# Kernel optimization log

Hardware: AMD Instinct MI355X
Metric: run time of the kernel (lower is better)

Reference implementation:

```python
import jax, jax.numpy as jnp
import numpy as np

# Fixed supermask = [3, 4, 16, 28, 0, 0, 0, 3]:
#   preproc: relu(Linear x3); l1 = GCN(x); l2 = GCN(l1); l3 = GCN(l2);
#   out = relu(Linear z3((l1+l2+l3)/3))
HIDDEN = 64


def gcn_conv(h, W, b, src, dst, norm, n_nodes):
    # PyG GCNConv: h' = scatter_add(norm * (hW)[src] -> dst) + b
    hw = h @ W                                  # [N, F]
    msg = hw[src] * norm[:, None]               # gather + scale  [E+N, F]
    agg = jax.ops.segment_sum(msg, dst, num_segments=n_nodes)
    return agg + b


def setup_inputs() -> dict:
    key = jax.random.key(0)
    ks = jax.random.split(key, 12)
    N, E, NFEAT, NCLASS = 100000, 1000000, 256, 40
    x = jax.random.normal(ks[0], (N, NFEAT), dtype=jnp.float32)
    edge_index = jax.random.randint(ks[1], (2, E), 0, N, dtype=jnp.int64)
    s = 1.0 / np.sqrt(NFEAT)
    h = 1.0 / np.sqrt(HIDDEN)
    return {
        "x": x,
        "edge_index": edge_index,
        "Wx": jax.random.uniform(ks[2], (NFEAT, HIDDEN), jnp.float32, -s, s),
        "bx": jnp.zeros((HIDDEN,), jnp.float32),
        "W1": jax.random.uniform(ks[3], (HIDDEN, HIDDEN), jnp.float32, -h, h),
        "b1": jnp.zeros((HIDDEN,), jnp.float32),
        "W2": jax.random.uniform(ks[4], (HIDDEN, HIDDEN), jnp.float32, -h, h),
        "b2": jnp.zeros((HIDDEN,), jnp.float32),
        "W3": jax.random.uniform(ks[5], (HIDDEN, HIDDEN), jnp.float32, -h, h),
        "b3": jnp.zeros((HIDDEN,), jnp.float32),
        "Wz": jax.random.uniform(ks[6], (HIDDEN, NCLASS), jnp.float32, -h, h),
        "bz": jnp.zeros((NCLASS,), jnp.float32),
    }


def reference(x, edge_index, Wx, bx, W1, b1, W2, b2, W3, b3, Wz, bz):
    n = x.shape[0]
    # add self-loops (PyG GCNConv default)
    loop = jnp.arange(n, dtype=edge_index.dtype)
    src = jnp.concatenate([edge_index[0], loop])
    dst = jnp.concatenate([edge_index[1], loop])
    deg = jax.ops.segment_sum(jnp.ones_like(dst, dtype=x.dtype), dst, num_segments=n)
    dinv = jnp.where(deg > 0, jax.lax.rsqrt(deg), 0.0)
    norm = dinv[src] * dinv[dst]                 # [E+N]

    h0 = jax.nn.relu(x @ Wx + bx)                # x_3(relu) o x3(Linear)
    l1 = gcn_conv(h0, W1, b1, src, dst, norm, n)
    l2 = gcn_conv(l1, W2, b2, src, dst, norm, n)
    l3 = gcn_conv(l2, W3, b3, src, dst, norm, n)
    z = (l1 + l2 + l3) / 3.0
    return jax.nn.relu(z @ Wz + bz)
```

## Files before the change

### kernel.cpp

```cpp
#include <hip/hip_runtime.h>

#define NFEAT 256
#define HID 64
#define NCLASS 40
#define EPB 4096
#define BCAP 8192

typedef _Float16 half8 __attribute__((ext_vector_type(8)));
typedef float floatx4 __attribute__((ext_vector_type(4)));

__device__ __forceinline__ void gld_lds16(const _Float16* g, _Float16* l) {
    __builtin_amdgcn_global_load_lds(
        (const __attribute__((address_space(1))) void*)g,
        (__attribute__((address_space(3))) void*)l, 16, 0, 0);
}

__global__ __launch_bounds__(256) void k_bin(const int* __restrict__ src, const int* __restrict__ dst,
                                             int* __restrict__ bcur, int* __restrict__ bwords,
                                             int nbuckets, int E, int nbin,
                                             const float* __restrict__ W1, const float* __restrict__ W2,
                                             const float* __restrict__ W3, _Float16* __restrict__ Wt16) {
    __shared__ int lcnt[256], loff[256], lcur[256], gbase[256], sc[256];
    __shared__ int sdst[EPB];
    __shared__ int words[EPB];
    int t = threadIdx.x;
    if (blockIdx.x >= (unsigned)nbin) {
        int l = blockIdx.x - nbin;
        const float* Ws = (l == 0) ? W1 : (l == 1) ? W2 : W3;
        _Float16* wt = Wt16 + l * 4096;
        for (int i = t; i < 4096; i += 256) {
            int col = i >> 6, k = i & 63;
            wt[i] = (_Float16)Ws[k * HID + col];
        }
        return;
    }
    int base = blockIdx.x * EPB;
    int n = E - base; if (n > EPB) n = EPB;
    lcnt[t] = 0;
    __syncthreads();
    for (int i = t; i < n; i += 256) {
        int d = dst[base + i];
        sdst[i] = d;
        atomicAdd(&lcnt[d >> 9], 1);
    }
    __syncthreads();
    int v = lcnt[t];
    sc[t] = v; __syncthreads();
    for (int o = 1; o < 256; o <<= 1) {
        int add = (t >= o) ? sc[t - o] : 0;
        __syncthreads();
        sc[t] += add;
        __syncthreads();
    }
    int excl = sc[t] - v;
    loff[t] = excl; lcur[t] = excl;
    __syncthreads();
    for (int i = t; i < n; i += 256) {
        int d = sdst[i], s = src[base + i];
        int b = d >> 9;
        int p = atomicAdd(&lcur[b], 1);
        words[p] = s | ((d & 511) << 17);
    }
    __syncthreads();
    if (t < nbuckets) {
        int c = lcnt[t];
        gbase[t] = c > 0 ? atomicAdd(&bcur[t], c) : 0;
    }
    __syncthreads();
    int lane = t & 63, wv = t >> 6;
    for (int b = wv; b < nbuckets; b += 4) {
        int o = loff[b], c = lcnt[b], gb = gbase[b];
        int* dstp = bwords + (size_t)b * BCAP;
        for (int i = lane; i < c; i += 64) {
            int gp = gb + i;
            if (gp < BCAP) dstp[gp] = words[o + i];
        }
    }
}

__global__ __launch_bounds__(256) void k_csr(const int* __restrict__ bcur, const int* __restrict__ bwords,
                                             int* __restrict__ csr, unsigned* __restrict__ pk,
                                             float* __restrict__ dinv, int N) {
    __shared__ int cnt[512], cur[512], sc[256];
    __shared__ int lcsr[BCAP];
    int t = threadIdx.x;
    int b = blockIdx.x;
    int nodebase = b << 9;
    int nb = bcur[b]; if (nb > BCAP) nb = BCAP;
    cnt[t] = 0; cnt[t + 256] = 0;
    __syncthreads();
    const int* wp = bwords + (size_t)b * BCAP;
    for (int i = t; i < nb; i += 256)
        atomicAdd(&cnt[wp[i] >> 17], 1);
    __syncthreads();
    int v0 = cnt[2 * t], v1 = cnt[2 * t + 1];
    int p = v0 + v1;
    sc[t] = p; __syncthreads();
    for (int o = 1; o < 256; o <<= 1) {
        int add = (t >= o) ? sc[t - o] : 0;
        __syncthreads();
        sc[t] += add;
        __syncthreads();
    }
    int e = sc[t] - p;
    cur[2 * t] = e; cur[2 * t + 1] = e + v0;
    #pragma unroll
    for (int j = 0; j < 2; ++j) {
        int node = nodebase + 2 * t + j;
        if (node < N) {
            int c = cnt[2 * t + j]; if (c > 2047) c = 2047;
            pk[node] = (unsigned)(b * BCAP + cur[2 * t + j]) | ((unsigned)c << 21);
            dinv[node] = rsqrtf((float)c + 1.0f);
        }
    }
    __syncthreads();
    for (int i = t; i < nb; i += 256) {
        int w = wp[i];
        int pos = atomicAdd(&cur[w >> 17], 1);
        lcsr[pos] = w & 0x1FFFF;
    }
    __syncthreads();
    int* cp = csr + (size_t)b * BCAP;
    for (int i = t; i < nb; i += 256) cp[i] = lcsr[i];
}

__global__ __launch_bounds__(512) void k_gemm_in(const float* __restrict__ x, const float* __restrict__ Wx,
                                                 const float* __restrict__ bx, _Float16* __restrict__ h0, int N) {
    __shared__ _Float16 Wt[64][264];
    int t = threadIdx.x;
    {
        int c = t & 63, k0 = (t >> 6) * 32;
        for (int k = k0; k < k0 + 32; ++k)
            Wt[c][k] = (_Float16)Wx[k * HID + c];
    }
    __syncthreads();
    int lane = t & 63, lg = lane >> 4, ln = lane & 15;
    int wid = (blockIdx.x * 512 + t) >> 6;
    int nw = (gridDim.x * 512) >> 6;
    float bb[4];
    #pragma unroll
    for (int g = 0; g < 4; ++g) bb[g] = bx[g * 16 + ln];
    int ntiles = N >> 4;
    for (int tile = wid; tile < ntiles; tile += nw) {
        int row0 = tile << 4;
        const float* xr = x + (size_t)(row0 + ln) * NFEAT + lg * 8;
        float4 av[16];
        #pragma unroll
        for (int ks = 0; ks < 8; ++ks) {
            av[2 * ks]     = *(const float4*)(xr + ks * 32);
            av[2 * ks + 1] = *(const float4*)(xr + ks * 32 + 4);
        }
        floatx4 acc[4] = {{0.f,0.f,0.f,0.f},{0.f,0.f,0.f,0.f},{0.f,0.f,0.f,0.f},{0.f,0.f,0.f,0.f}};
        #pragma unroll
        for (int ks = 0; ks < 8; ++ks) {
            float4 a0 = av[2 * ks], a1 = av[2 * ks + 1];
            half8 a;
            a[0]=(_Float16)a0.x; a[1]=(_Float16)a0.y; a[2]=(_Float16)a0.z; a[3]=(_Float16)a0.w;
            a[4]=(_Float16)a1.x; a[5]=(_Float16)a1.y; a[6]=(_Float16)a1.z; a[7]=(_Float16)a1.w;
            #pragma unroll
            for (int g = 0; g < 4; ++g) {
                half8 b = *(const half8*)&Wt[g * 16 + ln][ks * 32 + lg * 8];
                acc[g] = __builtin_amdgcn_mfma_f32_16x16x32_f16(a, b, acc[g], 0, 0, 0);
            }
        }
        #pragma unroll
        for (int g = 0; g < 4; ++g) {
            #pragma unroll
            for (int r = 0; r < 4; ++r) {
                int row = row0 + lg * 4 + r;
                h0[(size_t)row * HID + g * 16 + ln] = (_Float16)fmaxf(acc[g][r] + bb[g], 0.f);
            }
        }
    }
}

template<int WRN>
__global__ __launch_bounds__(256) void k_layer(const _Float16* __restrict__ Ph, const int* __restrict__ csr,
                                               const unsigned* __restrict__ pk, const float* __restrict__ dinv,
                                               const _Float16* __restrict__ Wt, const float* __restrict__ b,
                                               float* __restrict__ normf,
                                               _Float16* __restrict__ Lout, int N) {
    __shared__ _Float16 stage[4][8][8][64];
    __shared__ _Float16 z[32][72];
    _Float16 (*ot)[72] = (_Float16 (*)[72])&stage[0][0][0][0];
    int t = threadIdx.x;
    int lane = t & 63, wv = t >> 6;
    int sg = lane >> 3, f8 = lane & 7;
    int lg = lane >> 4, ln = lane & 15;
    int nb = blockIdx.x << 5;
    int node = nb + wv * 8 + sg;
    int nodec = node < N ? node : (N - 1);
    int col = wv * 16 + ln;
    half8 bf0 = *(const half8*)(Wt + col * 64 + lg * 8);
    half8 bf1 = *(const half8*)(Wt + col * 64 + 32 + lg * 8);
    float bb = b[col];

    unsigned pkv = (node < N) ? pk[node] : 0u;
    int off = (int)(pkv & 0x1FFFFFu);
    int c = (int)(pkv >> 21);
    float dd = (node < N) ? dinv[node] : 0.f;
    float acc[8];
    {
        half8 self = *(const half8*)(Ph + (size_t)nodec * HID + f8 * 8);
        float dd2 = dd * dd;
        #pragma unroll
        for (int j = 0; j < 8; ++j) acc[j] = (float)self[j] * dd2;
    }
    int cm = c;
    cm = max(cm, __shfl_xor(cm, 8));
    cm = max(cm, __shfl_xor(cm, 16));
    cm = max(cm, __shfl_xor(cm, 32));
    for (int jj = 0; jj < cm; jj += 8) {
        int e = jj + f8;
        bool ok = e < c;
        int s = nodec;
        float nm = 0.f;
        if (ok) {
            s = csr[off + e];
            if (WRN) {
                nm = dinv[s] * dd;
                normf[off + e] = nm;
            } else {
                nm = normf[off + e];
            }
        }
        #pragma unroll
        for (int j = 0; j < 8; ++j) {
            int ss = __shfl(s, j, 8);
            gld_lds16(Ph + (size_t)ss * HID + f8 * 8, &stage[wv][j][0][0]);
        }
        asm volatile("s_waitcnt vmcnt(0)" ::: "memory");
        #pragma unroll
        for (int j = 0; j < 8; ++j) {
            float nn = __shfl(nm, j, 8);
            half8 v = *(const half8*)&stage[wv][j][sg][f8 * 8];
            #pragma unroll
            for (int q = 0; q < 8; ++q) acc[q] = fmaf((float)v[q], nn, acc[q]);
        }
    }
    {
        half8 zv;
        #pragma unroll
        for (int j = 0; j < 8; ++j) zv[j] = (_Float16)acc[j];
        *(half8*)&z[wv * 8 + sg][f8 * 8] = zv;
    }
    __syncthreads();
    floatx4 acc0 = {0.f, 0.f, 0.f, 0.f}, acc1 = {0.f, 0.f, 0.f, 0.f};
    {
        half8 a0 = *(const half8*)&z[ln][lg * 8];
        half8 a1 = *(const half8*)&z[16 + ln][lg * 8];
        acc0 = __builtin_amdgcn_mfma_f32_16x16x32_f16(a0, bf0, acc0, 0, 0, 0);
        acc1 = __builtin_amdgcn_mfma_f32_16x16x32_f16(a1, bf0, acc1, 0, 0, 0);
        a0 = *(const half8*)&z[ln][32 + lg * 8];
        a1 = *(const half8*)&z[16 + ln][32 + lg * 8];
        acc0 = __builtin_amdgcn_mfma_f32_16x16x32_f16(a0, bf1, acc0, 0, 0, 0);
        acc1 = __builtin_amdgcn_mfma_f32_16x16x32_f16(a1, bf1, acc1, 0, 0, 0);
    }
    #pragma unroll
    for (int r = 0; r < 4; ++r) {
        ot[lg * 4 + r][wv * 16 + ln] = (_Float16)(acc0[r] + bb);
        ot[16 + lg * 4 + r][wv * 16 + ln] = (_Float16)(acc1[r] + bb);
    }
    __syncthreads();
    {
        int row = t >> 3, c8 = t & 7;
        int onode = nb + row;
        if (onode < N)
            *(half8*)(Lout + (size_t)onode * HID + c8 * 8) = *(const half8*)&ot[row][c8 * 8];
    }
}

__global__ __launch_bounds__(256) void k_gemm_out(const _Float16* __restrict__ L1, const _Float16* __restrict__ L2,
                                                  const _Float16* __restrict__ L3, const float* __restrict__ Wz,
                                                  const float* __restrict__ bz, float* __restrict__ outp, int N) {
    int t = threadIdx.x;
    int lane = t & 63, lg = lane >> 4, ln = lane & 15;
    int wid = (blockIdx.x * 256 + t) >> 6;
    int nw = (gridDim.x * 256) >> 6;
    half8 b[2][3];
    float bb[3];
    #pragma unroll
    for (int g = 0; g < 3; ++g) {
        int col = g * 16 + ln;
        bb[g] = (col < NCLASS) ? bz[col] : 0.f;
        #pragma unroll
        for (int ks = 0; ks < 2; ++ks)
            #pragma unroll
            for (int j = 0; j < 8; ++j)
                b[ks][g][j] = (col < NCLASS) ? (_Float16)(Wz[(ks * 32 + lg * 8 + j) * NCLASS + col] * (1.f / 3.f)) : (_Float16)0.f;
    }
    int ntiles = N >> 4;
    for (int tile = wid; tile < ntiles; tile += nw) {
        int row0 = tile << 4;
        size_t rb = (size_t)(row0 + ln) * HID + lg * 8;
        floatx4 acc[3] = {{0.f,0.f,0.f,0.f},{0.f,0.f,0.f,0.f},{0.f,0.f,0.f,0.f}};
        #pragma unroll
        for (int ks = 0; ks < 2; ++ks) {
            half8 a1 = *(const half8*)(L1 + rb + ks * 32);
            half8 a2 = *(const half8*)(L2 + rb + ks * 32);
            half8 a3 = *(const half8*)(L3 + rb + ks * 32);
            half8 a;
            #pragma unroll
            for (int j = 0; j < 8; ++j)
                a[j] = (_Float16)((float)a1[j] + (float)a2[j] + (float)a3[j]);
            #pragma unroll
            for (int g = 0; g < 3; ++g)
                acc[g] = __builtin_amdgcn_mfma_f32_16x16x32_f16(a, b[ks][g], acc[g], 0, 0, 0);
        }
        #pragma unroll
        for (int g = 0; g < 3; ++g) {
            int col = g * 16 + ln;
            if (col < NCLASS) {
                #pragma unroll
                for (int r = 0; r < 4; ++r)
                    outp[(size_t)(row0 + lg * 4 + r) * NCLASS + col] = fmaxf(acc[g][r] + bb[g], 0.f);
            }
        }
    }
}

extern "C" void kernel_launch(void* const* d_in, const int* in_sizes, int n_in,
                              void* d_out, int out_size, void* d_ws, size_t ws_size,
                              hipStream_t stream) {
    const float* x  = (const float*)d_in[0];
    const int*   ei = (const int*)d_in[1];
    const float* Wx = (const float*)d_in[2];
    const float* bx = (const float*)d_in[3];
    const float* W1 = (const float*)d_in[4];
    const float* b1 = (const float*)d_in[5];
    const float* W2 = (const float*)d_in[6];
    const float* b2 = (const float*)d_in[7];
    const float* W3 = (const float*)d_in[8];
    const float* b3 = (const float*)d_in[9];
    const float* Wz = (const float*)d_in[10];
    const float* bz = (const float*)d_in[11];
    float* out = (float*)d_out;

    int N = in_sizes[0] / NFEAT;
    int E = in_sizes[1] / 2;
    const int* src = ei;
    const int* dst = ei + E;
    int nbuckets = (N + 511) >> 9;

    size_t nh = (size_t)N * HID;
    size_t Npad = ((size_t)N + 7) / 8 * 8;
    int*      bcur = (int*)d_ws;
    float*    dinv = (float*)d_ws + 256;
    unsigned* pk   = (unsigned*)(dinv + Npad);
    _Float16* H0   = (_Float16*)(pk + Npad);
    _Float16* L1   = H0 + nh;
    _Float16* L2   = L1 + nh;
    _Float16* L3   = L2 + nh;
    int*      bwords = (int*)(L3 + nh);
    int*      csr  = bwords + (size_t)nbuckets * BCAP;
    _Float16* Wt16 = (_Float16*)(csr + (size_t)nbuckets * BCAP);
    float*    normf = (float*)(Wt16 + 3 * 4096);

    int nbin = (E + EPB - 1) / EPB;
    hipMemsetAsync(bcur, 0, 256 * sizeof(int), stream);
    k_bin<<<nbin + 3, 256, 0, stream>>>(src, dst, bcur, bwords, nbuckets, E, nbin, W1, W2, W3, Wt16);
    k_csr<<<nbuckets, 256, 0, stream>>>(bcur, bwords, csr, pk, dinv, N);

    k_gemm_in<<<256, 512, 0, stream>>>(x, Wx, bx, H0, N);

    int layer_blocks = (N + 31) / 32;
    k_layer<1><<<layer_blocks, 256, 0, stream>>>(H0, csr, pk, dinv, Wt16,          b1, normf, L1, N);
    k_layer<0><<<layer_blocks, 256, 0, stream>>>(L1, csr, pk, dinv, Wt16 + 4096,   b2, normf, L2, N);
    k_layer<0><<<layer_blocks, 256, 0, stream>>>(L2, csr, pk, dinv, Wt16 + 8192,   b3, normf, L3, N);

    k_gemm_out<<<512, 256, 0, stream>>>(L1, L2, L3, Wz, bz, out, N);
}
```

Measured before the change: 333.0 us.

## Fuse input GEMM into binning kernel and prefetch edges in layer gather

The input linear layer (x@Wx+relu) moves into the edge-binning kernel as extra blocks, so binning and the dense GEMM run concurrently in one launch and a kernel boundary disappears. In the GCN layer kernel, the gather via global_load_lds into an LDS staging buffer with a full vmcnt(0) wait is replaced by direct global half8 loads. The next chunk's csr index and norm are software-prefetched, and the loop bound is each node's own degree instead of the wave maximum. This trades LDS staging for more in-flight register loads and drops the per-wave max-degree reduction.

```diff
diff --git a/kernel.cpp b/kernel.cpp
--- a/kernel.cpp
+++ b/kernel.cpp
@@ -9,23 +9,26 @@
 typedef _Float16 half8 __attribute__((ext_vector_type(8)));
 typedef float floatx4 __attribute__((ext_vector_type(4)));
 
-__device__ __forceinline__ void gld_lds16(const _Float16* g, _Float16* l) {
-    __builtin_amdgcn_global_load_lds(
-        (const __attribute__((address_space(1))) void*)g,
-        (__attribute__((address_space(3))) void*)l, 16, 0, 0);
-}
-
-__global__ __launch_bounds__(256) void k_bin(const int* __restrict__ src, const int* __restrict__ dst,
+struct BinSM {
+    int lcnt[256], loff[256], lcur[256], gbase[256], sc[256];
+    int sdst[EPB];
+    int words[EPB];
+};
+
+__global__ __launch_bounds__(256) void k_pre(const int* __restrict__ src, const int* __restrict__ dst,
                                              int* __restrict__ bcur, int* __restrict__ bwords,
                                              int nbuckets, int E, int nbin,
                                              const float* __restrict__ W1, const float* __restrict__ W2,
-                                             const float* __restrict__ W3, _Float16* __restrict__ Wt16) {
-    __shared__ int lcnt[256], loff[256], lcur[256], gbase[256], sc[256];
-    __shared__ int sdst[EPB];
-    __shared__ int words[EPB];
+                                             const float* __restrict__ W3, _Float16* __restrict__ Wt16,
+                                             const float* __restrict__ x, const float* __restrict__ Wx,
+                                             const float* __restrict__ bx, _Float16* __restrict__ h0,
+                                             int N, int ngemm) {
+    __shared__ __align__(16) char smraw[sizeof(BinSM)];
     int t = threadIdx.x;
-    if (blockIdx.x >= (unsigned)nbin) {
-        int l = blockIdx.x - nbin;
+    int bid = blockIdx.x;
+
+    if (bid >= nbin && bid < nbin + 3) {
+        int l = bid - nbin;
         const float* Ws = (l == 0) ? W1 : (l == 1) ? W2 : W3;
         _Float16* wt = Wt16 + l * 4096;
         for (int i = t; i < 4096; i += 256) {
@@ -34,46 +37,99 @@
         }
         return;
     }
-    int base = blockIdx.x * EPB;
+
+    if (bid >= nbin + 3) {
+        _Float16 (*Wt)[264] = (_Float16 (*)[264])smraw;
+        {
+            int c = t & 63, k0 = (t >> 6) * 64;
+            for (int k = k0; k < k0 + 64; ++k)
+                Wt[c][k] = (_Float16)Wx[k * HID + c];
+        }
+        __syncthreads();
+        int lane = t & 63, wv = t >> 6;
+        int lg = lane >> 4, ln = lane & 15;
+        int gb = bid - nbin - 3;
+        int wid = gb * 4 + wv;
+        int nw = ngemm * 4;
+        float bb[4];
+        #pragma unroll
+        for (int g = 0; g < 4; ++g) bb[g] = bx[g * 16 + ln];
+        int ntiles = N >> 4;
+        for (int tile = wid; tile < ntiles; tile += nw) {
+            int row0 = tile << 4;
+            const float* xr = x + (size_t)(row0 + ln) * NFEAT + lg * 8;
+            float4 av[16];
+            #pragma unroll
+            for (int ks = 0; ks < 8; ++ks) {
+                av[2 * ks]     = *(const float4*)(xr + ks * 32);
+                av[2 * ks + 1] = *(const float4*)(xr + ks * 32 + 4);
+            }
+            floatx4 acc[4] = {{0.f,0.f,0.f,0.f},{0.f,0.f,0.f,0.f},{0.f,0.f,0.f,0.f},{0.f,0.f,0.f,0.f}};
+            #pragma unroll
+            for (int ks = 0; ks < 8; ++ks) {
+                float4 a0 = av[2 * ks], a1 = av[2 * ks + 1];
+                half8 a;
+                a[0]=(_Float16)a0.x; a[1]=(_Float16)a0.y; a[2]=(_Float16)a0.z; a[3]=(_Float16)a0.w;
+                a[4]=(_Float16)a1.x; a[5]=(_Float16)a1.y; a[6]=(_Float16)a1.z; a[7]=(_Float16)a1.w;
+                #pragma unroll
+                for (int g = 0; g < 4; ++g) {
+                    half8 b = *(const half8*)&Wt[g * 16 + ln][ks * 32 + lg * 8];
+                    acc[g] = __builtin_amdgcn_mfma_f32_16x16x32_f16(a, b, acc[g], 0, 0, 0);
+                }
+            }
+            #pragma unroll
+            for (int g = 0; g < 4; ++g) {
+                #pragma unroll
+                for (int r = 0; r < 4; ++r) {
+                    int row = row0 + lg * 4 + r;
+                    h0[(size_t)row * HID + g * 16 + ln] = (_Float16)fmaxf(acc[g][r] + bb[g], 0.f);
+                }
+            }
+        }
+        return;
+    }
+
+    BinSM* sm = (BinSM*)smraw;
+    int base = bid * EPB;
     int n = E - base; if (n > EPB) n = EPB;
-    lcnt[t] = 0;
+    sm->lcnt[t] = 0;
     __syncthreads();
     for (int i = t; i < n; i += 256) {
         int d = dst[base + i];
-        sdst[i] = d;
-        atomicAdd(&lcnt[d >> 9], 1);
-    }
-    __syncthreads();
-    int v = lcnt[t];
-    sc[t] = v; __syncthreads();
+        sm->sdst[i] = d;
+        atomicAdd(&sm->lcnt[d >> 9], 1);
+    }
+    __syncthreads();
+    int v = sm->lcnt[t];
+    sm->sc[t] = v; __syncthreads();
     for (int o = 1; o < 256; o <<= 1) {
-        int add = (t >= o) ? sc[t - o] : 0;
-        __syncthreads();
-        sc[t] += add;
-        __syncthreads();
-    }
-    int excl = sc[t] - v;
-    loff[t] = excl; lcur[t] = excl;
+        int add = (t >= o) ? sm->sc[t - o] : 0;
+        __syncthreads();
+        sm->sc[t] += add;
+        __syncthreads();
+    }
+    int excl = sm->sc[t] - v;
+    sm->loff[t] = excl; sm->lcur[t] = excl;
     __syncthreads();
     for (int i = t; i < n; i += 256) {
-        int d = sdst[i], s = src[base + i];
+        int d = sm->sdst[i], s = src[base + i];
         int b = d >> 9;
-        int p = atomicAdd(&lcur[b], 1);
-        words[p] = s | ((d & 511) << 17);
+        int p = atomicAdd(&sm->lcur[b], 1);
+        sm->words[p] = s | ((d & 511) << 17);
     }
     __syncthreads();
     if (t < nbuckets) {
-        int c = lcnt[t];
-        gbase[t] = c > 0 ? atomicAdd(&bcur[t], c) : 0;
+        int c = sm->lcnt[t];
+        sm->gbase[t] = c > 0 ? atomicAdd(&bcur[t], c) : 0;
     }
     __syncthreads();
     int lane = t & 63, wv = t >> 6;
     for (int b = wv; b < nbuckets; b += 4) {
-        int o = loff[b], c = lcnt[b], gb = gbase[b];
+        int o = sm->loff[b], c = sm->lcnt[b], gb = sm->gbase[b];
         int* dstp = bwords + (size_t)b * BCAP;
         for (int i = lane; i < c; i += 64) {
             int gp = gb + i;
-            if (gp < BCAP) dstp[gp] = words[o + i];
+            if (gp < BCAP) dstp[gp] = sm->words[o + i];
         }
     }
 }
@@ -124,119 +180,69 @@
     for (int i = t; i < nb; i += 256) cp[i] = lcsr[i];
 }
 
-__global__ __launch_bounds__(512) void k_gemm_in(const float* __restrict__ x, const float* __restrict__ Wx,
-                                                 const float* __restrict__ bx, _Float16* __restrict__ h0, int N) {
-    __shared__ _Float16 Wt[64][264];
-    int t = threadIdx.x;
-    {
-        int c = t & 63, k0 = (t >> 6) * 32;
-        for (int k = k0; k < k0 + 32; ++k)
-            Wt[c][k] = (_Float16)Wx[k * HID + c];
-    }
-    __syncthreads();
-    int lane = t & 63, lg = lane >> 4, ln = lane & 15;
-    int wid = (blockIdx.x * 512 + t) >> 6;
-    int nw = (gridDim.x * 512) >> 6;
-    float bb[4];
-    #pragma unroll
-    for (int g = 0; g < 4; ++g) bb[g] = bx[g * 16 + ln];
-    int ntiles = N >> 4;
-    for (int tile = wid; tile < ntiles; tile += nw) {
-        int row0 = tile << 4;
-        const float* xr = x + (size_t)(row0 + ln) * NFEAT + lg * 8;
-        float4 av[16];
-        #pragma unroll
-        for (int ks = 0; ks < 8; ++ks) {
-            av[2 * ks]     = *(const float4*)(xr + ks * 32);
-            av[2 * ks + 1] = *(const float4*)(xr + ks * 32 + 4);
-        }
-        floatx4 acc[4] = {{0.f,0.f,0.f,0.f},{0.f,0.f,0.f,0.f},{0.f,0.f,0.f,0.f},{0.f,0.f,0.f,0.f}};
-        #pragma unroll
-        for (int ks = 0; ks < 8; ++ks) {
-            float4 a0 = av[2 * ks], a1 = av[2 * ks + 1];
-            half8 a;
-            a[0]=(_Float16)a0.x; a[1]=(_Float16)a0.y; a[2]=(_Float16)a0.z; a[3]=(_Float16)a0.w;
-            a[4]=(_Float16)a1.x; a[5]=(_Float16)a1.y; a[6]=(_Float16)a1.z; a[7]=(_Float16)a1.w;
-            #pragma unroll
-            for (int g = 0; g < 4; ++g) {
-                half8 b = *(const half8*)&Wt[g * 16 + ln][ks * 32 + lg * 8];
-                acc[g] = __builtin_amdgcn_mfma_f32_16x16x32_f16(a, b, acc[g], 0, 0, 0);
-            }
-        }
-        #pragma unroll
-        for (int g = 0; g < 4; ++g) {
-            #pragma unroll
-            for (int r = 0; r < 4; ++r) {
-                int row = row0 + lg * 4 + r;
-                h0[(size_t)row * HID + g * 16 + ln] = (_Float16)fmaxf(acc[g][r] + bb[g], 0.f);
-            }
-        }
-    }
-}
-
 template<int WRN>
 __global__ __launch_bounds__(256) void k_layer(const _Float16* __restrict__ Ph, const int* __restrict__ csr,
                                                const unsigned* __restrict__ pk, const float* __restrict__ dinv,
                                                const _Float16* __restrict__ Wt, const float* __restrict__ b,
                                                float* __restrict__ normf,
                                                _Float16* __restrict__ Lout, int N) {
-    __shared__ _Float16 stage[4][8][8][64];
     __shared__ _Float16 z[32][72];
-    _Float16 (*ot)[72] = (_Float16 (*)[72])&stage[0][0][0][0];
+    __shared__ _Float16 ot[32][72];
     int t = threadIdx.x;
     int lane = t & 63, wv = t >> 6;
     int sg = lane >> 3, f8 = lane & 7;
     int lg = lane >> 4, ln = lane & 15;
     int nb = blockIdx.x << 5;
     int node = nb + wv * 8 + sg;
-    int nodec = node < N ? node : (N - 1);
+    bool valid = node < N;
+    int nodec = valid ? node : (N - 1);
     int col = wv * 16 + ln;
     half8 bf0 = *(const half8*)(Wt + col * 64 + lg * 8);
     half8 bf1 = *(const half8*)(Wt + col * 64 + 32 + lg * 8);
     float bb = b[col];
 
-    unsigned pkv = (node < N) ? pk[node] : 0u;
+    unsigned pkv = valid ? pk[node] : 0u;
     int off = (int)(pkv & 0x1FFFFFu);
     int c = (int)(pkv >> 21);
-    float dd = (node < N) ? dinv[node] : 0.f;
+    float dd = valid ? dinv[node] : 0.f;
+    const _Float16* pb = Ph + f8 * 8;
     float acc[8];
     {
-        half8 self = *(const half8*)(Ph + (size_t)nodec * HID + f8 * 8);
+        half8 self = *(const half8*)(pb + (size_t)nodec * HID);
         float dd2 = dd * dd;
         #pragma unroll
         for (int j = 0; j < 8; ++j) acc[j] = (float)self[j] * dd2;
     }
-    int cm = c;
-    cm = max(cm, __shfl_xor(cm, 8));
-    cm = max(cm, __shfl_xor(cm, 16));
-    cm = max(cm, __shfl_xor(cm, 32));
-    for (int jj = 0; jj < cm; jj += 8) {
-        int e = jj + f8;
-        bool ok = e < c;
-        int s = nodec;
-        float nm = 0.f;
-        if (ok) {
-            s = csr[off + e];
-            if (WRN) {
-                nm = dinv[s] * dd;
-                normf[off + e] = nm;
-            } else {
-                nm = normf[off + e];
-            }
+    int ecur = f8;
+    bool ok = ecur < c;
+    int s_cur = ok ? csr[off + ecur] : nodec;
+    float nm_cur;
+    if (WRN) {
+        nm_cur = ok ? dinv[s_cur] * dd : 0.f;
+        if (ok) normf[off + ecur] = nm_cur;
+    } else {
+        nm_cur = ok ? normf[off + ecur] : 0.f;
+    }
+    for (int jj = 0; jj < c; jj += 8) {
+        int en = jj + 8 + f8;
+        bool okn = en < c;
+        int s_nxt = okn ? csr[off + en] : nodec;
+        float nm_nxt;
+        if (WRN) {
+            nm_nxt = okn ? dinv[s_nxt] * dd : 0.f;
+            if (okn) normf[off + en] = nm_nxt;
+        } else {
+            nm_nxt = okn ? normf[off + en] : 0.f;
         }
         #pragma unroll
         for (int j = 0; j < 8; ++j) {
-            int ss = __shfl(s, j, 8);
-            gld_lds16(Ph + (size_t)ss * HID + f8 * 8, &stage[wv][j][0][0]);
-        }
-        asm volatile("s_waitcnt vmcnt(0)" ::: "memory");
-        #pragma unroll
-        for (int j = 0; j < 8; ++j) {
-            float nn = __shfl(nm, j, 8);
-            half8 v = *(const half8*)&stage[wv][j][sg][f8 * 8];
+            int ss = __shfl(s_cur, j, 8);
+            float nn = __shfl(nm_cur, j, 8);
+            half8 v = *(const half8*)(pb + (size_t)ss * HID);
             #pragma unroll
             for (int q = 0; q < 8; ++q) acc[q] = fmaf((float)v[q], nn, acc[q]);
         }
+        s_cur = s_nxt; nm_cur = nm_nxt;
     }
     {
         half8 zv;
@@ -357,11 +363,11 @@
     float*    normf = (float*)(Wt16 + 3 * 4096);
 
     int nbin = (E + EPB - 1) / EPB;
+    int ngemm = 512;
     hipMemsetAsync(bcur, 0, 256 * sizeof(int), stream);
-    k_bin<<<nbin + 3, 256, 0, stream>>>(src, dst, bcur, bwords, nbuckets, E, nbin, W1, W2, W3, Wt16);
+    k_pre<<<nbin + 3 + ngemm, 256, 0, stream>>>(src, dst, bcur, bwords, nbuckets, E, nbin,
+                                                W1, W2, W3, Wt16, x, Wx, bx, H0, N, ngemm);
     k_csr<<<nbuckets, 256, 0, stream>>>(bcur, bwords, csr, pk, dinv, N);
-
-    k_gemm_in<<<256, 512, 0, stream>>>(x, Wx, bx, H0, N);
 
     int layer_blocks = (N + 31) / 32;
     k_layer<1><<<layer_blocks, 256, 0, stream>>>(H0, csr, pk, dinv, Wt16,          b1, normf, L1, N);
```

Result: faster. 285.2 us (-14.3%).
